# Kernel optimization log

Measured on AMD Instinct MI355X. Metric: run time of the kernel, lower is better.

Reference implementation:

```python
import jax, jax.numpy as jnp
import numpy as np
from jax import lax

W_R, W_C, W_P, W_S = 1.0, 0.5, 1.0, 0.1
EPS_NORM = 1e-12  # F.normalize eps
EPS_CLAMP = 1e-07


def _conv(x, w, pad):
    return lax.conv_general_dilated(x, w, (1, 1), pad,
                                    dimension_numbers=('NCHW', 'OIHW', 'NCHW'))


def _dir_kernels():
    # (4 out, 3 in, 1, 3): left, right, up, down exactly as in the torch module
    k = np.zeros((4, 3, 1, 3), np.float32)
    k[0, 1, 0] = [-1, 1, 0]   # kernel_left  (green channel only)
    k[1, 1, 0] = [0, 1, -1]   # kernel_right (green channel only)
    k[2, 0, 0] = [0, -1, 0]   # kernel_up: -R center
    k[2, 1, 0] = [0, 1, 0]    #            +G center
    k[3, 1, 0] = [0, 1, 0]    # kernel_down: +G center
    k[3, 2, 0] = [0, -1, 0]   #              -B center
    return jnp.asarray(k)


def _mfn_loss(a, b):
    # --- reconstruction (L1) ---
    r_loss = jnp.mean(jnp.abs(a - b))

    # --- color loss: per-pixel, normalize each (B,C) slice along batch dim ---
    an = a / jnp.maximum(jnp.linalg.norm(a, axis=0, keepdims=True), EPS_NORM)
    bn = b / jnp.maximum(jnp.linalg.norm(b, axis=0, keepdims=True), EPS_NORM)
    cos = jnp.sum(an * bn, axis=(0, 1))  # [H, W]
    cos = jnp.clip(cos, -1.0 + EPS_CLAMP, 1.0 - EPS_CLAMP)
    c_loss = jnp.sum(jnp.arccos(cos))

    # --- smoothness: Sobel on first image of batch, per RGB channel ---
    sobel = jnp.array([[1, 0, -1], [2, 0, -2], [1, 0, -1]],
                      jnp.float32).reshape(1, 1, 3, 3)
    ga = _conv(a[0][:, None], sobel, [(1, 1), (1, 1)])  # (3,1,H,W)
    gb = _conv(b[0][:, None], sobel, [(1, 1), (1, 1)])
    s_loss = jnp.sum(jnp.abs(ga - gb))

    # --- spatial consistency: 4x4 avg-pool then 4 directional 1x3 convs ---
    pool = lambda x: lax.reduce_window(x, 0.0, lax.add,
                                       (1, 1, 4, 4), (1, 1, 4, 4), 'VALID') / 16.0
    ap, bp = pool(a), pool(b)
    kern = _dir_kernels()
    # conv is linear: D_inp_* - D_enh_* = conv(bp - ap)
    d = _conv(bp - ap, kern, [(0, 0), (1, 1)])  # (B,4,h,w)
    p_loss = jnp.mean(jnp.sum(d * d, axis=1))

    return W_C * c_loss + W_R * r_loss + W_P * p_loss + W_S * s_loss


def setup_inputs() -> dict:
    key = jax.random.key(0)
    k1, k2 = jax.random.split(key)
    B, C, H, W = 8, 3, 1024, 1024
    predictions = jax.random.uniform(k1, (B, C, H, W), jnp.float32)
    targets = jax.random.uniform(k2, (B, C, H, W), jnp.float32)
    return {"predictions": predictions, "targets": targets}


def reference(predictions, targets):
    return _mfn_loss(predictions, targets)
```

## Files before the change

kernel.cpp:

```cpp
#include <hip/hip_runtime.h>
#include <math.h>

#define HW1 (1024 * 1024)
#define WID 1024
#define HEI 1024
#define NMAIN 512
#define NSOB  384
#define NBLK  (NMAIN + NSOB)

typedef float f32x4 __attribute__((ext_vector_type(4)));

__device__ __forceinline__ void block_atomic_add(float v, float* target, volatile float* sdata) {
#pragma unroll
    for (int off = 32; off > 0; off >>= 1)
        v += __shfl_down(v, off, 64);
    const int lane = threadIdx.x & 63;
    const int wv   = threadIdx.x >> 6;
    if (lane == 0) sdata[wv] = v;
    __syncthreads();
    if (threadIdx.x == 0) {
        float s = 0.f;
        for (int i = 0; i < 4; ++i) s += sdata[i];
        atomicAdd(target, s);
    }
    __syncthreads();
}

__global__ __launch_bounds__(256) void k_A(const float* __restrict__ A,
                                           const float* __restrict__ B,
                                           float* __restrict__ acc) {
    __shared__ float pd[8][3][4][130];
    __shared__ float s1[4];

    const int tid = threadIdx.x;

    if (blockIdx.x < NMAIN) {
        const int gy = blockIdx.x >> 1;
        const int h  = blockIdx.x & 1;
        const int xl = tid & 63;
        const int yl = tid >> 6;
        const int y  = gy * 4 + yl;
        const int rbase = y * 256 + h * 128;

        const f32x4* A4 = reinterpret_cast<const f32x4*>(A);
        const f32x4* B4 = reinterpret_cast<const f32x4*>(B);

        float na2[3][8], nb2[3][8], dt[3][8];
#pragma unroll
        for (int c = 0; c < 3; ++c)
#pragma unroll
            for (int j = 0; j < 8; ++j) { na2[c][j] = 0.f; nb2[c][j] = 0.f; dt[c][j] = 0.f; }
        float r_sum = 0.f;

#pragma unroll 2
        for (int b = 0; b < 8; ++b) {
#pragma unroll
            for (int c = 0; c < 3; ++c) {
                const int pbase = (b * 3 + c) * (HW1 / 4) + rbase;
                const f32x4 a0 = A4[pbase + xl];
                const f32x4 a1 = A4[pbase + 64 + xl];
                const f32x4 b0 = B4[pbase + xl];
                const f32x4 b1 = B4[pbase + 64 + xl];
                float pd0 = 0.f, pd1 = 0.f;
#pragma unroll
                for (int j = 0; j < 4; ++j) {
                    const float a = a0[j], t = b0[j];
                    na2[c][j] += a * a; nb2[c][j] += t * t; dt[c][j] += a * t;
                    r_sum += fabsf(a - t); pd0 += t - a;
                }
#pragma unroll
                for (int j = 0; j < 4; ++j) {
                    const float a = a1[j], t = b1[j];
                    na2[c][4 + j] += a * a; nb2[c][4 + j] += t * t; dt[c][4 + j] += a * t;
                    r_sum += fabsf(a - t); pd1 += t - a;
                }
                pd[b][c][yl][1 + xl]  = pd0;
                pd[b][c][yl][65 + xl] = pd1;
            }
        }

        if (tid < 192) {
            const int side = tid & 1;
            const int yl2  = (tid >> 1) & 3;
            const int c2   = (tid >> 3) % 3;
            const int b2   = tid / 24;
            const int dataside = (h == 0) ? 1 : 0;
            if (!(c2 == 1 && side == dataside))
                pd[b2][c2][yl2][side ? 129 : 0] = 0.f;
        } else if (tid < 224) {
            const int i2  = tid - 192;
            const int b2  = i2 >> 2;
            const int yl2 = i2 & 3;
            const int gcol = (h == 0) ? 128 : 127;
            const int slot = (h == 0) ? 129 : 0;
            const int gp = (b2 * 3 + 1) * (HW1 / 4) + (gy * 4 + yl2) * 256 + gcol;
            const f32x4 ga = A4[gp];
            const f32x4 gb = B4[gp];
            pd[b2][1][yl2][slot] = (gb[0] - ga[0]) + (gb[1] - ga[1])
                                 + (gb[2] - ga[2]) + (gb[3] - ga[3]);
        }

        float c_sum = 0.f;
#pragma unroll
        for (int j = 0; j < 8; ++j) {
            float cs = 0.f;
#pragma unroll
            for (int c = 0; c < 3; ++c) {
                const float na = fmaxf(sqrtf(na2[c][j]), 1e-12f);
                const float nb = fmaxf(sqrtf(nb2[c][j]), 1e-12f);
                cs += dt[c][j] / (na * nb);
            }
            cs = fminf(fmaxf(cs, -1.0f + 1e-7f), 1.0f - 1e-7f);
            c_sum += acosf(cs);
        }

        __syncthreads();

        float p_sum = 0.f;
#pragma unroll
        for (int i = 0; i < 4; ++i) {
            const int item = i * 256 + tid;
            const int b2 = item >> 7;
            const int x  = item & 127;
            float g = 0.f, gl = 0.f, gr = 0.f, rr = 0.f, bb = 0.f;
#pragma unroll
            for (int yy = 0; yy < 4; ++yy) {
                g  += pd[b2][1][yy][1 + x];
                gl += pd[b2][1][yy][x];
                gr += pd[b2][1][yy][2 + x];
                rr += pd[b2][0][yy][1 + x];
                bb += pd[b2][2][yy][1 + x];
            }
            const float d0 = g - gl;
            const float d1 = g - gr;
            const float d2 = g - rr;
            const float d3 = g - bb;
            p_sum += d0 * d0 + d1 * d1 + d2 * d2 + d3 * d3;
        }
        p_sum *= (1.0f / 256.0f);

        block_atomic_add(r_sum, acc + 0, s1);
        block_atomic_add(c_sum, acc + 1, s1);
        block_atomic_add(p_sum, acc + 3, s1);
    } else {
        const int t   = (blockIdx.x - NMAIN) * 256 + tid;
        const int xt  = t & 127;
        const int rem = t >> 7;
        const int yt  = rem & 255;
        const int c   = rem >> 8;
        const int x0  = xt * 8;
        const int y0  = yt * 4;

        const float* Ap = A + (size_t)c * HW1;
        const float* Bp = B + (size_t)c * HW1;

        float rd[6][8];
#pragma unroll
        for (int r = 0; r < 6; ++r) {
            const int yy = y0 - 1 + r;
            if (yy < 0 || yy >= HEI) {
#pragma unroll
                for (int j = 0; j < 8; ++j) rd[r][j] = 0.f;
                continue;
            }
            const float* ap = Ap + (size_t)yy * WID;
            const float* bp = Bp + (size_t)yy * WID;
            const float4 a4 = *reinterpret_cast<const float4*>(ap + x0);
            const float4 a5 = *reinterpret_cast<const float4*>(ap + x0 + 4);
            const float4 b4 = *reinterpret_cast<const float4*>(bp + x0);
            const float4 b5 = *reinterpret_cast<const float4*>(bp + x0 + 4);
            const float dm = (x0 > 0)    ? (ap[x0 - 1] - bp[x0 - 1]) : 0.f;
            const float dp = (x0 < 1016) ? (ap[x0 + 8] - bp[x0 + 8]) : 0.f;
            const float d0 = a4.x - b4.x, d1 = a4.y - b4.y, d2 = a4.z - b4.z, d3 = a4.w - b4.w;
            const float d4 = a5.x - b5.x, d5 = a5.y - b5.y, d6 = a5.z - b5.z, d7 = a5.w - b5.w;
            rd[r][0] = dm - d1;
            rd[r][1] = d0 - d2;
            rd[r][2] = d1 - d3;
            rd[r][3] = d2 - d4;
            rd[r][4] = d3 - d5;
            rd[r][5] = d4 - d6;
            rd[r][6] = d5 - d7;
            rd[r][7] = d6 - dp;
        }

        float s_sum = 0.f;
#pragma unroll
        for (int o = 0; o < 4; ++o)
#pragma unroll
            for (int j = 0; j < 8; ++j)
                s_sum += fabsf(rd[o][j] + 2.f * rd[o + 1][j] + rd[o + 2][j]);

        block_atomic_add(s_sum, acc + 2, s1);
    }
}

__global__ void k_final(const float* __restrict__ acc, float* __restrict__ out) {
    const float r = acc[0] * (1.0f / 25165824.0f);
    const float c = acc[1];
    const float s = acc[2];
    const float p = acc[3] * (1.0f / 524288.0f);
    out[0] = 0.5f * c + 1.0f * r + 1.0f * p + 0.1f * s;
}

extern "C" void kernel_launch(void* const* d_in, const int* in_sizes, int n_in,
                              void* d_out, int out_size, void* d_ws, size_t ws_size,
                              hipStream_t stream) {
    const float* A = (const float*)d_in[0];
    const float* B = (const float*)d_in[1];
    float* acc = (float*)d_ws;

    hipMemsetAsync(acc, 0, 64 * sizeof(float), stream);
    hipLaunchKernelGGL(k_A,     dim3(NBLK), dim3(256), 0, stream, A, B, acc);
    hipLaunchKernelGGL(k_final, dim3(1),    dim3(1),   0, stream, acc, (float*)d_out);
}
```

Baseline: 63.38 us.

## Fuse Sobel smoothness pass into main blocks via shared-memory fp16 halo tile

Removes the separate Sobel block group and computes the batch-0 Sobel gradient inside each main block. Batch-0 differences from the main loads go into an fp16 shared tile, and only the halo rows and columns are loaded from global memory. The pooled-difference buffer is also switched to fp16 so both shared arrays fit. This avoids re-reading batch-0 data and cuts the launch to 512 blocks, but fp16 storage lowers the precision of the smoothness and pooling terms, and each block does more serial work.

```diff
diff --git a/kernel.cpp b/kernel.cpp
--- a/kernel.cpp
+++ b/kernel.cpp
@@ -5,10 +5,9 @@
 #define WID 1024
 #define HEI 1024
 #define NMAIN 512
-#define NSOB  384
-#define NBLK  (NMAIN + NSOB)
 
 typedef float f32x4 __attribute__((ext_vector_type(4)));
+typedef _Float16 f16;
 
 __device__ __forceinline__ void block_atomic_add(float v, float* target, volatile float* sdata) {
 #pragma unroll
@@ -29,169 +28,195 @@
 __global__ __launch_bounds__(256) void k_A(const float* __restrict__ A,
                                            const float* __restrict__ B,
                                            float* __restrict__ acc) {
-    __shared__ float pd[8][3][4][130];
+    __shared__ f16 pd[8][3][4][130];
+    __shared__ f16 dsh[3][6][528];
     __shared__ float s1[4];
 
     const int tid = threadIdx.x;
-
-    if (blockIdx.x < NMAIN) {
-        const int gy = blockIdx.x >> 1;
-        const int h  = blockIdx.x & 1;
-        const int xl = tid & 63;
-        const int yl = tid >> 6;
-        const int y  = gy * 4 + yl;
-        const int rbase = y * 256 + h * 128;
-
-        const f32x4* A4 = reinterpret_cast<const f32x4*>(A);
-        const f32x4* B4 = reinterpret_cast<const f32x4*>(B);
-
-        float na2[3][8], nb2[3][8], dt[3][8];
-#pragma unroll
-        for (int c = 0; c < 3; ++c)
-#pragma unroll
-            for (int j = 0; j < 8; ++j) { na2[c][j] = 0.f; nb2[c][j] = 0.f; dt[c][j] = 0.f; }
-        float r_sum = 0.f;
+    const int gy = blockIdx.x >> 1;
+    const int h  = blockIdx.x & 1;
+    const int xl = tid & 63;
+    const int yl = tid >> 6;
+    const int y  = gy * 4 + yl;
+    const int rbase = y * 256 + h * 128;
+
+    const f32x4* A4 = reinterpret_cast<const f32x4*>(A);
+    const f32x4* B4 = reinterpret_cast<const f32x4*>(B);
+
+    {
+        unsigned* dz = reinterpret_cast<unsigned*>(&dsh[0][0][0]);
+        for (int i = tid; i < 3 * 6 * 528 / 2; i += 256) dz[i] = 0u;
+    }
+    __syncthreads();
+
+    float na2[3][8], nb2[3][8], dt[3][8];
+#pragma unroll
+    for (int c = 0; c < 3; ++c)
+#pragma unroll
+        for (int j = 0; j < 8; ++j) { na2[c][j] = 0.f; nb2[c][j] = 0.f; dt[c][j] = 0.f; }
+    float r_sum = 0.f;
+
+#pragma unroll
+    for (int c = 0; c < 3; ++c) {
+        const int pbase = c * (HW1 / 4) + rbase;
+        const f32x4 a0 = A4[pbase + xl];
+        const f32x4 a1 = A4[pbase + 64 + xl];
+        const f32x4 b0 = B4[pbase + xl];
+        const f32x4 b1 = B4[pbase + 64 + xl];
+        float pd0 = 0.f, pd1 = 0.f;
+#pragma unroll
+        for (int j = 0; j < 4; ++j) {
+            const float a = a0[j], t = b0[j];
+            na2[c][j] += a * a; nb2[c][j] += t * t; dt[c][j] += a * t;
+            r_sum += fabsf(a - t); pd0 += t - a;
+            dsh[c][yl + 1][8 + 4 * xl + j] = (f16)(a - t);
+        }
+#pragma unroll
+        for (int j = 0; j < 4; ++j) {
+            const float a = a1[j], t = b1[j];
+            na2[c][4 + j] += a * a; nb2[c][4 + j] += t * t; dt[c][4 + j] += a * t;
+            r_sum += fabsf(a - t); pd1 += t - a;
+            dsh[c][yl + 1][8 + 256 + 4 * xl + j] = (f16)(a - t);
+        }
+        pd[0][c][yl][1 + xl]  = (f16)pd0;
+        pd[0][c][yl][65 + xl] = (f16)pd1;
+    }
 
 #pragma unroll 2
-        for (int b = 0; b < 8; ++b) {
-#pragma unroll
-            for (int c = 0; c < 3; ++c) {
-                const int pbase = (b * 3 + c) * (HW1 / 4) + rbase;
-                const f32x4 a0 = A4[pbase + xl];
-                const f32x4 a1 = A4[pbase + 64 + xl];
-                const f32x4 b0 = B4[pbase + xl];
-                const f32x4 b1 = B4[pbase + 64 + xl];
-                float pd0 = 0.f, pd1 = 0.f;
-#pragma unroll
-                for (int j = 0; j < 4; ++j) {
-                    const float a = a0[j], t = b0[j];
-                    na2[c][j] += a * a; nb2[c][j] += t * t; dt[c][j] += a * t;
-                    r_sum += fabsf(a - t); pd0 += t - a;
-                }
-#pragma unroll
-                for (int j = 0; j < 4; ++j) {
-                    const float a = a1[j], t = b1[j];
-                    na2[c][4 + j] += a * a; nb2[c][4 + j] += t * t; dt[c][4 + j] += a * t;
-                    r_sum += fabsf(a - t); pd1 += t - a;
-                }
-                pd[b][c][yl][1 + xl]  = pd0;
-                pd[b][c][yl][65 + xl] = pd1;
+    for (int b = 1; b < 8; ++b) {
+#pragma unroll
+        for (int c = 0; c < 3; ++c) {
+            const int pbase = (b * 3 + c) * (HW1 / 4) + rbase;
+            const f32x4 a0 = A4[pbase + xl];
+            const f32x4 a1 = A4[pbase + 64 + xl];
+            const f32x4 b0 = B4[pbase + xl];
+            const f32x4 b1 = B4[pbase + 64 + xl];
+            float pd0 = 0.f, pd1 = 0.f;
+#pragma unroll
+            for (int j = 0; j < 4; ++j) {
+                const float a = a0[j], t = b0[j];
+                na2[c][j] += a * a; nb2[c][j] += t * t; dt[c][j] += a * t;
+                r_sum += fabsf(a - t); pd0 += t - a;
             }
-        }
-
-        if (tid < 192) {
-            const int side = tid & 1;
-            const int yl2  = (tid >> 1) & 3;
-            const int c2   = (tid >> 3) % 3;
-            const int b2   = tid / 24;
-            const int dataside = (h == 0) ? 1 : 0;
-            if (!(c2 == 1 && side == dataside))
-                pd[b2][c2][yl2][side ? 129 : 0] = 0.f;
-        } else if (tid < 224) {
-            const int i2  = tid - 192;
-            const int b2  = i2 >> 2;
-            const int yl2 = i2 & 3;
-            const int gcol = (h == 0) ? 128 : 127;
-            const int slot = (h == 0) ? 129 : 0;
-            const int gp = (b2 * 3 + 1) * (HW1 / 4) + (gy * 4 + yl2) * 256 + gcol;
+#pragma unroll
+            for (int j = 0; j < 4; ++j) {
+                const float a = a1[j], t = b1[j];
+                na2[c][4 + j] += a * a; nb2[c][4 + j] += t * t; dt[c][4 + j] += a * t;
+                r_sum += fabsf(a - t); pd1 += t - a;
+            }
+            pd[b][c][yl][1 + xl]  = (f16)pd0;
+            pd[b][c][yl][65 + xl] = (f16)pd1;
+        }
+    }
+
+    if (tid < 192) {
+        const int side = tid & 1;
+        const int yl2  = (tid >> 1) & 3;
+        const int c2   = (tid >> 3) % 3;
+        const int b2   = tid / 24;
+        const int dataside = (h == 0) ? 1 : 0;
+        if (!(c2 == 1 && side == dataside))
+            pd[b2][c2][yl2][side ? 129 : 0] = (f16)0.f;
+    } else if (tid < 224) {
+        const int i2  = tid - 192;
+        const int b2  = i2 >> 2;
+        const int yl2 = i2 & 3;
+        const int gcol = (h == 0) ? 128 : 127;
+        const int slot = (h == 0) ? 129 : 0;
+        const int gp = (b2 * 3 + 1) * (HW1 / 4) + (gy * 4 + yl2) * 256 + gcol;
+        const f32x4 ga = A4[gp];
+        const f32x4 gb = B4[gp];
+        pd[b2][1][yl2][slot] = (f16)((gb[0] - ga[0]) + (gb[1] - ga[1])
+                                   + (gb[2] - ga[2]) + (gb[3] - ga[3]));
+    }
+
+    for (int i = tid; i < 804; i += 256) {
+        int c2, r2, f4, yy;
+        if (i < 780) {
+            const int f_rel = i % 130;
+            const int rc    = i / 130;
+            const int rr    = rc & 1;
+            c2 = rc >> 1;
+            r2 = rr ? 5 : 0;
+            f4 = h * 128 - 1 + f_rel;
+            yy = rr ? (gy * 4 + 4) : (gy * 4 - 1);
+        } else {
+            const int i2 = i - 780;
+            const int side = i2 & 1;
+            const int yl2  = (i2 >> 1) & 3;
+            c2 = i2 >> 3;
+            r2 = yl2 + 1;
+            f4 = h * 128 + (side ? 128 : -1);
+            yy = gy * 4 + yl2;
+        }
+        if (f4 >= 0 && f4 < 256 && yy >= 0 && yy < HEI) {
+            const int gp = c2 * (HW1 / 4) + yy * 256 + f4;
             const f32x4 ga = A4[gp];
             const f32x4 gb = B4[gp];
-            pd[b2][1][yl2][slot] = (gb[0] - ga[0]) + (gb[1] - ga[1])
-                                 + (gb[2] - ga[2]) + (gb[3] - ga[3]);
-        }
-
-        float c_sum = 0.f;
-#pragma unroll
-        for (int j = 0; j < 8; ++j) {
-            float cs = 0.f;
-#pragma unroll
-            for (int c = 0; c < 3; ++c) {
-                const float na = fmaxf(sqrtf(na2[c][j]), 1e-12f);
-                const float nb = fmaxf(sqrtf(nb2[c][j]), 1e-12f);
-                cs += dt[c][j] / (na * nb);
-            }
-            cs = fminf(fmaxf(cs, -1.0f + 1e-7f), 1.0f - 1e-7f);
-            c_sum += acosf(cs);
-        }
-
-        __syncthreads();
-
-        float p_sum = 0.f;
-#pragma unroll
-        for (int i = 0; i < 4; ++i) {
-            const int item = i * 256 + tid;
-            const int b2 = item >> 7;
-            const int x  = item & 127;
-            float g = 0.f, gl = 0.f, gr = 0.f, rr = 0.f, bb = 0.f;
-#pragma unroll
-            for (int yy = 0; yy < 4; ++yy) {
-                g  += pd[b2][1][yy][1 + x];
-                gl += pd[b2][1][yy][x];
-                gr += pd[b2][1][yy][2 + x];
-                rr += pd[b2][0][yy][1 + x];
-                bb += pd[b2][2][yy][1 + x];
-            }
-            const float d0 = g - gl;
-            const float d1 = g - gr;
-            const float d2 = g - rr;
-            const float d3 = g - bb;
-            p_sum += d0 * d0 + d1 * d1 + d2 * d2 + d3 * d3;
-        }
-        p_sum *= (1.0f / 256.0f);
-
-        block_atomic_add(r_sum, acc + 0, s1);
-        block_atomic_add(c_sum, acc + 1, s1);
-        block_atomic_add(p_sum, acc + 3, s1);
-    } else {
-        const int t   = (blockIdx.x - NMAIN) * 256 + tid;
-        const int xt  = t & 127;
-        const int rem = t >> 7;
-        const int yt  = rem & 255;
-        const int c   = rem >> 8;
-        const int x0  = xt * 8;
-        const int y0  = yt * 4;
-
-        const float* Ap = A + (size_t)c * HW1;
-        const float* Bp = B + (size_t)c * HW1;
-
-        float rd[6][8];
-#pragma unroll
-        for (int r = 0; r < 6; ++r) {
-            const int yy = y0 - 1 + r;
-            if (yy < 0 || yy >= HEI) {
-#pragma unroll
-                for (int j = 0; j < 8; ++j) rd[r][j] = 0.f;
-                continue;
-            }
-            const float* ap = Ap + (size_t)yy * WID;
-            const float* bp = Bp + (size_t)yy * WID;
-            const float4 a4 = *reinterpret_cast<const float4*>(ap + x0);
-            const float4 a5 = *reinterpret_cast<const float4*>(ap + x0 + 4);
-            const float4 b4 = *reinterpret_cast<const float4*>(bp + x0);
-            const float4 b5 = *reinterpret_cast<const float4*>(bp + x0 + 4);
-            const float dm = (x0 > 0)    ? (ap[x0 - 1] - bp[x0 - 1]) : 0.f;
-            const float dp = (x0 < 1016) ? (ap[x0 + 8] - bp[x0 + 8]) : 0.f;
-            const float d0 = a4.x - b4.x, d1 = a4.y - b4.y, d2 = a4.z - b4.z, d3 = a4.w - b4.w;
-            const float d4 = a5.x - b5.x, d5 = a5.y - b5.y, d6 = a5.z - b5.z, d7 = a5.w - b5.w;
-            rd[r][0] = dm - d1;
-            rd[r][1] = d0 - d2;
-            rd[r][2] = d1 - d3;
-            rd[r][3] = d2 - d4;
-            rd[r][4] = d3 - d5;
-            rd[r][5] = d4 - d6;
-            rd[r][6] = d5 - d7;
-            rd[r][7] = d6 - dp;
-        }
-
-        float s_sum = 0.f;
-#pragma unroll
-        for (int o = 0; o < 4; ++o)
-#pragma unroll
-            for (int j = 0; j < 8; ++j)
-                s_sum += fabsf(rd[o][j] + 2.f * rd[o + 1][j] + rd[o + 2][j]);
-
-        block_atomic_add(s_sum, acc + 2, s1);
-    }
+            const int sbase = 4 * (f4 - 128 * h) + 8;
+#pragma unroll
+            for (int j = 0; j < 4; ++j)
+                dsh[c2][r2][sbase + j] = (f16)(ga[j] - gb[j]);
+        }
+    }
+
+    float c_sum = 0.f;
+#pragma unroll
+    for (int j = 0; j < 8; ++j) {
+        float cs = 0.f;
+#pragma unroll
+        for (int c = 0; c < 3; ++c) {
+            const float na = fmaxf(sqrtf(na2[c][j]), 1e-12f);
+            const float nb = fmaxf(sqrtf(nb2[c][j]), 1e-12f);
+            cs += dt[c][j] / (na * nb);
+        }
+        cs = fminf(fmaxf(cs, -1.0f + 1e-7f), 1.0f - 1e-7f);
+        c_sum += acosf(cs);
+    }
+
+    __syncthreads();
+
+    float p_sum = 0.f;
+#pragma unroll
+    for (int i = 0; i < 4; ++i) {
+        const int item = i * 256 + tid;
+        const int b2 = item >> 7;
+        const int x  = item & 127;
+        float g = 0.f, gl = 0.f, gr = 0.f, rr = 0.f, bb = 0.f;
+#pragma unroll
+        for (int yy = 0; yy < 4; ++yy) {
+            g  += (float)pd[b2][1][yy][1 + x];
+            gl += (float)pd[b2][1][yy][x];
+            gr += (float)pd[b2][1][yy][2 + x];
+            rr += (float)pd[b2][0][yy][1 + x];
+            bb += (float)pd[b2][2][yy][1 + x];
+        }
+        const float d0 = g - gl;
+        const float d1 = g - gr;
+        const float d2 = g - rr;
+        const float d3 = g - bb;
+        p_sum += d0 * d0 + d1 * d1 + d2 * d2 + d3 * d3;
+    }
+    p_sum *= (1.0f / 256.0f);
+
+    float s_sum = 0.f;
+#pragma unroll
+    for (int i = 0; i < 24; ++i) {
+        const int idx = i * 256 + tid;
+        const int c2  = idx >> 11;
+        const int row = (idx >> 9) & 3;
+        const int col = idx & 511;
+        const int s0  = col + 8;
+        const float rd0 = (float)dsh[c2][row][s0 - 1]     - (float)dsh[c2][row][s0 + 1];
+        const float rd1 = (float)dsh[c2][row + 1][s0 - 1] - (float)dsh[c2][row + 1][s0 + 1];
+        const float rd2 = (float)dsh[c2][row + 2][s0 - 1] - (float)dsh[c2][row + 2][s0 + 1];
+        s_sum += fabsf(rd0 + 2.f * rd1 + rd2);
+    }
+
+    block_atomic_add(r_sum, acc + 0, s1);
+    block_atomic_add(c_sum, acc + 1, s1);
+    block_atomic_add(s_sum, acc + 2, s1);
+    block_atomic_add(p_sum, acc + 3, s1);
 }
 
 __global__ void k_final(const float* __restrict__ acc, float* __restrict__ out) {
@@ -210,6 +235,6 @@
     float* acc = (float*)d_ws;
 
     hipMemsetAsync(acc, 0, 64 * sizeof(float), stream);
-    hipLaunchKernelGGL(k_A,     dim3(NBLK), dim3(256), 0, stream, A, B, acc);
-    hipLaunchKernelGGL(k_final, dim3(1),    dim3(1),   0, stream, acc, (float*)d_out);
-}
+    hipLaunchKernelGGL(k_A,     dim3(NMAIN), dim3(256), 0, stream, A, B, acc);
+    hipLaunchKernelGGL(k_final, dim3(1),     dim3(1),   0, stream, acc, (float*)d_out);
+}
```

Result: slower. 67.05 us (+5.8%).

## Split main tiles into quarter-width blocks and store pooled diffs as fp16

Applied to the files above, without the earlier changes.

Doubles the number of main blocks so each covers 64 float4 columns instead of 128. This halves per-thread accumulators and loads and adds halo loads on both sides of each tile. The shared pooled-difference buffer is shrunk and stored as half precision to cut LDS use and raise occupancy. The fp16 storage adds rounding error to the spatial-consistency term, and the extra halo loads and more atomics are added overhead.

```diff
diff --git a/kernel.cpp b/kernel.cpp
--- a/kernel.cpp
+++ b/kernel.cpp
@@ -4,11 +4,12 @@
 #define HW1 (1024 * 1024)
 #define WID 1024
 #define HEI 1024
-#define NMAIN 512
+#define NMAIN 1024
 #define NSOB  384
 #define NBLK  (NMAIN + NSOB)
 
 typedef float f32x4 __attribute__((ext_vector_type(4)));
+typedef _Float16 f16;
 
 __device__ __forceinline__ void block_atomic_add(float v, float* target, volatile float* sdata) {
 #pragma unroll
@@ -29,27 +30,27 @@
 __global__ __launch_bounds__(256) void k_A(const float* __restrict__ A,
                                            const float* __restrict__ B,
                                            float* __restrict__ acc) {
-    __shared__ float pd[8][3][4][130];
+    __shared__ f16 pdl[8][3][4][66];
     __shared__ float s1[4];
 
     const int tid = threadIdx.x;
 
     if (blockIdx.x < NMAIN) {
-        const int gy = blockIdx.x >> 1;
-        const int h  = blockIdx.x & 1;
+        const int gy = blockIdx.x >> 2;
+        const int q  = blockIdx.x & 3;
         const int xl = tid & 63;
         const int yl = tid >> 6;
         const int y  = gy * 4 + yl;
-        const int rbase = y * 256 + h * 128;
+        const int rbase = y * 256 + q * 64;
 
         const f32x4* A4 = reinterpret_cast<const f32x4*>(A);
         const f32x4* B4 = reinterpret_cast<const f32x4*>(B);
 
-        float na2[3][8], nb2[3][8], dt[3][8];
+        float na2[3][4], nb2[3][4], dt[3][4];
 #pragma unroll
         for (int c = 0; c < 3; ++c)
 #pragma unroll
-            for (int j = 0; j < 8; ++j) { na2[c][j] = 0.f; nb2[c][j] = 0.f; dt[c][j] = 0.f; }
+            for (int j = 0; j < 4; ++j) { na2[c][j] = 0.f; nb2[c][j] = 0.f; dt[c][j] = 0.f; }
         float r_sum = 0.f;
 
 #pragma unroll 2
@@ -58,51 +59,36 @@
             for (int c = 0; c < 3; ++c) {
                 const int pbase = (b * 3 + c) * (HW1 / 4) + rbase;
                 const f32x4 a0 = A4[pbase + xl];
-                const f32x4 a1 = A4[pbase + 64 + xl];
                 const f32x4 b0 = B4[pbase + xl];
-                const f32x4 b1 = B4[pbase + 64 + xl];
-                float pd0 = 0.f, pd1 = 0.f;
+                float pd0 = 0.f;
 #pragma unroll
                 for (int j = 0; j < 4; ++j) {
                     const float a = a0[j], t = b0[j];
                     na2[c][j] += a * a; nb2[c][j] += t * t; dt[c][j] += a * t;
                     r_sum += fabsf(a - t); pd0 += t - a;
                 }
-#pragma unroll
-                for (int j = 0; j < 4; ++j) {
-                    const float a = a1[j], t = b1[j];
-                    na2[c][4 + j] += a * a; nb2[c][4 + j] += t * t; dt[c][4 + j] += a * t;
-                    r_sum += fabsf(a - t); pd1 += t - a;
-                }
-                pd[b][c][yl][1 + xl]  = pd0;
-                pd[b][c][yl][65 + xl] = pd1;
-            }
-        }
-
-        if (tid < 192) {
+                pdl[b][c][yl][1 + xl] = (f16)pd0;
+            }
+        }
+
+        if (tid < 64) {
+            const int b2   = tid >> 3;
+            const int yl2  = (tid >> 1) & 3;
             const int side = tid & 1;
-            const int yl2  = (tid >> 1) & 3;
-            const int c2   = (tid >> 3) % 3;
-            const int b2   = tid / 24;
-            const int dataside = (h == 0) ? 1 : 0;
-            if (!(c2 == 1 && side == dataside))
-                pd[b2][c2][yl2][side ? 129 : 0] = 0.f;
-        } else if (tid < 224) {
-            const int i2  = tid - 192;
-            const int b2  = i2 >> 2;
-            const int yl2 = i2 & 3;
-            const int gcol = (h == 0) ? 128 : 127;
-            const int slot = (h == 0) ? 129 : 0;
-            const int gp = (b2 * 3 + 1) * (HW1 / 4) + (gy * 4 + yl2) * 256 + gcol;
-            const f32x4 ga = A4[gp];
-            const f32x4 gb = B4[gp];
-            pd[b2][1][yl2][slot] = (gb[0] - ga[0]) + (gb[1] - ga[1])
-                                 + (gb[2] - ga[2]) + (gb[3] - ga[3]);
+            const int f4   = q * 64 + (side ? 64 : -1);
+            float pg = 0.f;
+            if (f4 >= 0 && f4 < 256) {
+                const int gp = (b2 * 3 + 1) * (HW1 / 4) + (gy * 4 + yl2) * 256 + f4;
+                const f32x4 ga = A4[gp];
+                const f32x4 gb = B4[gp];
+                pg = (gb[0] - ga[0]) + (gb[1] - ga[1]) + (gb[2] - ga[2]) + (gb[3] - ga[3]);
+            }
+            pdl[b2][1][yl2][side ? 65 : 0] = (f16)pg;
         }
 
         float c_sum = 0.f;
 #pragma unroll
-        for (int j = 0; j < 8; ++j) {
+        for (int j = 0; j < 4; ++j) {
             float cs = 0.f;
 #pragma unroll
             for (int c = 0; c < 3; ++c) {
@@ -118,18 +104,18 @@
 
         float p_sum = 0.f;
 #pragma unroll
-        for (int i = 0; i < 4; ++i) {
+        for (int i = 0; i < 2; ++i) {
             const int item = i * 256 + tid;
-            const int b2 = item >> 7;
-            const int x  = item & 127;
+            const int b2 = item >> 6;
+            const int x  = item & 63;
             float g = 0.f, gl = 0.f, gr = 0.f, rr = 0.f, bb = 0.f;
 #pragma unroll
             for (int yy = 0; yy < 4; ++yy) {
-                g  += pd[b2][1][yy][1 + x];
-                gl += pd[b2][1][yy][x];
-                gr += pd[b2][1][yy][2 + x];
-                rr += pd[b2][0][yy][1 + x];
-                bb += pd[b2][2][yy][1 + x];
+                g  += (float)pdl[b2][1][yy][1 + x];
+                gl += (float)pdl[b2][1][yy][x];
+                gr += (float)pdl[b2][1][yy][2 + x];
+                rr += (float)pdl[b2][0][yy][1 + x];
+                bb += (float)pdl[b2][2][yy][1 + x];
             }
             const float d0 = g - gl;
             const float d1 = g - gr;
```

Result: slower. 88.30 us (+39.3%).
